# Kernel tuning notes

Measured on AMD Instinct MI355X. Metric: run time of the kernel, lower is better.

The kernel has to match this reference:

```python
import jax, jax.numpy as jnp
import numpy as np

BETA = 0.25
SK_EPSILONS = [0.0, 0.0, 0.003]
SK_ITERS = 50
B_SIZE = 262144
LATENT_DIM = 32
K = 256


def setup_inputs() -> dict:
    key = jax.random.key(0)
    kz, k0, k1, k2 = jax.random.split(key, 4)
    return {
        "z": jax.random.normal(kz, (B_SIZE, LATENT_DIM), dtype=jnp.float32),
        "cb0": jax.random.normal(k0, (K, LATENT_DIM), dtype=jnp.float32),
        "cb1": jax.random.normal(k1, (K, LATENT_DIM), dtype=jnp.float32),
        "cb2": jax.random.normal(k2, (K, LATENT_DIM), dtype=jnp.float32),
    }


def _sq_dists(residual, codebook):
    # ||r - c||^2 = ||r||^2 + ||c||^2 - 2 r.c  -> (B, K), avoids (B,K,D) broadcast
    r2 = jnp.sum(residual * residual, axis=1, keepdims=True)      # (B,1)
    c2 = jnp.sum(codebook * codebook, axis=1)                     # (K,)
    cross = residual @ codebook.T                                 # (B,K)
    return r2 + c2 - 2.0 * cross


def _sinkhorn(d_centered, epsilon, n_iters):
    # log-domain Sinkhorn-Knopp, matches torch reference
    B, Kk = d_centered.shape
    log_B = jnp.log(jnp.asarray(B, dtype=d_centered.dtype))
    log_K = jnp.log(jnp.asarray(Kk, dtype=d_centered.dtype))
    log_Q = -d_centered / epsilon
    log_Q = log_Q - jax.scipy.special.logsumexp(log_Q)

    def body(_, lq):
        lq = lq - jax.scipy.special.logsumexp(lq, axis=1, keepdims=True) - log_B
        lq = lq - jax.scipy.special.logsumexp(lq, axis=0, keepdims=True) - log_K
        return lq

    log_Q = jax.lax.fori_loop(0, n_iters, body, log_Q)
    return jnp.exp(log_Q + log_B)


def _quantize_level(residual, codebook, sk_epsilon, use_sk=True):
    dists = _sq_dists(residual, codebook)  # (B, K)
    codes_argmin = jnp.argmin(dists, axis=-1)
    if use_sk and sk_epsilon > 0:
        d = jax.lax.stop_gradient(dists)
        d_max = jnp.max(d)
        d_min = jnp.min(d)
        mid = (d_max + d_min) / 2
        amp = jnp.maximum(d_max - mid, 1e-05)
        Q = _sinkhorn((d - mid) / amp, sk_epsilon, SK_ITERS)
        bad = jnp.any(jnp.isnan(Q)) | jnp.any(jnp.isinf(Q))
        codes = jnp.where(bad, codes_argmin, jnp.argmax(Q, axis=-1))
    else:
        codes = codes_argmin
    quantized = codebook[codes]  # (B, D) gather
    return codes, quantized


def reference(z, cb0, cb1, cb2):
    codebooks = [cb0, cb1, cb2]
    sg = jax.lax.stop_gradient
    residual = z
    all_codes = []
    quantized_total = jnp.zeros_like(z)
    rq_loss = jnp.asarray(0.0, dtype=z.dtype)
    for codebook, sk_epsilon in zip(codebooks, SK_EPSILONS):
        codes, e = _quantize_level(residual, codebook, sk_epsilon, use_sk=True)
        all_codes.append(codes)
        rq_loss = rq_loss + jnp.mean((sg(residual) - e) ** 2)
        rq_loss = rq_loss + BETA * jnp.mean((residual - sg(e)) ** 2)
        e_st = residual + sg(e - residual)  # straight-through
        quantized_total = quantized_total + e_st
        residual = residual - sg(e)
    return (all_codes[0], all_codes[1], all_codes[2], quantized_total, rq_loss)
```

## Files before the change

### kernel.cpp

```cpp
#include <hip/hip_runtime.h>


#define BSZ   262144
#define DIM   32
#define KK    256
#define CHUNK 128
#define NBLK  (BSZ / CHUNK)
#define NIBLK (BSZ / 256)
#define LROW  36
#define SKEPS 0.003f
#define NIT   50

#define WS_SSQ  0
#define WS_MINK 1
#define WS_MAXK 2
#define WS_TWOT 3
#define WS_W0   256
#define WS_WA   512
#define WS_C2   1024
#define WSB_SIG 8192
#define WSB_BH  32768
#define WSB_BL  49152
#define WSB_QB  65536

#define OC0   0
#define OC1   BSZ
#define OC2   (2 * BSZ)
#define OQ    (3 * BSZ)
#define OLOSS (3 * BSZ + BSZ * DIM)
#define OU_AH (3u * BSZ)
#define OU_AL (3u * BSZ + 4194304u)

typedef short short8 __attribute__((ext_vector_type(8)));
typedef _Float16 half8 __attribute__((ext_vector_type(8)));
typedef float f32x4 __attribute__((ext_vector_type(4)));

#if __has_builtin(__builtin_amdgcn_exp2f)
#define EXP2(x) __builtin_amdgcn_exp2f(x)
#else
#define EXP2(x) exp2f(x)
#endif

#if __has_builtin(__builtin_amdgcn_update_dpp)
#define ROR16(x, N)                                                            \
  __int_as_float(__builtin_amdgcn_update_dpp(__float_as_int(x),                \
                 __float_as_int(x), 0x120 + (N), 0xF, 0xF, false))
#define ROR16I(x, N) __builtin_amdgcn_update_dpp((x), (x), 0x120 + (N), 0xF, 0xF, false)
#else
#define ROR16(x, N) __shfl_xor((x), (N))
#define ROR16I(x, N) __shfl_xor((x), (N))
#endif

__device__ __forceinline__ float wred_sum(float x) {
  x += ROR16(x, 1); x += ROR16(x, 2); x += ROR16(x, 4); x += ROR16(x, 8);
  x += __shfl_xor(x, 16); x += __shfl_xor(x, 32);
  return x;
}
__device__ __forceinline__ float wred_max(float x) {
  x = fmaxf(x, ROR16(x, 1)); x = fmaxf(x, ROR16(x, 2));
  x = fmaxf(x, ROR16(x, 4)); x = fmaxf(x, ROR16(x, 8));
  x = fmaxf(x, __shfl_xor(x, 16)); x = fmaxf(x, __shfl_xor(x, 32));
  return x;
}
__device__ __forceinline__ float wred_min(float x) {
  x = fminf(x, ROR16(x, 1)); x = fminf(x, ROR16(x, 2));
  x = fminf(x, ROR16(x, 4)); x = fminf(x, ROR16(x, 8));
  x = fminf(x, __shfl_xor(x, 16)); x = fminf(x, __shfl_xor(x, 32));
  return x;
}
__device__ __forceinline__ float g16_max(float x) {
  x = fmaxf(x, ROR16(x, 1)); x = fmaxf(x, ROR16(x, 2));
  x = fmaxf(x, ROR16(x, 4)); x = fmaxf(x, ROR16(x, 8));
  return x;
}
__device__ __forceinline__ float g16_sum(float x) {
  x += ROR16(x, 1); x += ROR16(x, 2); x += ROR16(x, 4); x += ROR16(x, 8);
  return x;
}
__device__ __forceinline__ void g16_argmax(float& v, int& j) {
  { float ov = ROR16(v,1); int oj = ROR16I(j,1); if (ov > v || (ov == v && oj < j)) { v = ov; j = oj; } }
  { float ov = ROR16(v,2); int oj = ROR16I(j,2); if (ov > v || (ov == v && oj < j)) { v = ov; j = oj; } }
  { float ov = ROR16(v,4); int oj = ROR16I(j,4); if (ov > v || (ov == v && oj < j)) { v = ov; j = oj; } }
  { float ov = ROR16(v,8); int oj = ROR16I(j,8); if (ov > v || (ov == v && oj < j)) { v = ov; j = oj; } }
}

__device__ __forceinline__ unsigned fkey(float f) {
  unsigned b = __float_as_uint(f);
  return (b & 0x80000000u) ? ~b : (b | 0x80000000u);
}
__device__ __forceinline__ float fkeyinv(unsigned k) {
  return __uint_as_float((k & 0x80000000u) ? (k ^ 0x80000000u) : ~k);
}
__device__ __forceinline__ unsigned pk2h(_Float16 a, _Float16 b) {
  unsigned short ua = __builtin_bit_cast(unsigned short, a);
  unsigned short ub = __builtin_bit_cast(unsigned short, b);
  return (unsigned)ua | ((unsigned)ub << 16);
}
__device__ __forceinline__ unsigned short bf16rne(float x) {
  unsigned u = __float_as_uint(x);
  return (unsigned short)((u + 0x7FFFu + ((u >> 16) & 1u)) >> 16);
}
__device__ __forceinline__ float bf2f(unsigned short h) {
  return __uint_as_float(((unsigned)h) << 16);
}
__device__ __forceinline__ void split3_8(const float* xs, short8& a1, short8& a2, short8& a3) {
#pragma unroll
  for (int u = 0; u < 8; ++u) {
    float x = xs[u];
    unsigned short b1 = bf16rne(x); x -= bf2f(b1);
    unsigned short b2 = bf16rne(x); x -= bf2f(b2);
    unsigned short b3 = bf16rne(x);
    a1[u] = (short)b1; a2[u] = (short)b2; a3[u] = (short)b3;
  }
}
__device__ __forceinline__ f32x4 mfma6r(short8 A1, short8 A2, short8 A3,
                                        short8 B1, short8 B2, short8 B3, f32x4 acc) {
  acc = __builtin_amdgcn_mfma_f32_16x16x32_bf16(A3, B1, acc, 0, 0, 0);
  acc = __builtin_amdgcn_mfma_f32_16x16x32_bf16(A1, B3, acc, 0, 0, 0);
  acc = __builtin_amdgcn_mfma_f32_16x16x32_bf16(A2, B2, acc, 0, 0, 0);
  acc = __builtin_amdgcn_mfma_f32_16x16x32_bf16(A2, B1, acc, 0, 0, 0);
  acc = __builtin_amdgcn_mfma_f32_16x16x32_bf16(A1, B2, acc, 0, 0, 0);
  acc = __builtin_amdgcn_mfma_f32_16x16x32_bf16(A1, B1, acc, 0, 0, 0);
  return acc;
}
__device__ __forceinline__ void build_a(const float* zl, int b, int lane,
                                        short8& A1, short8& A2, short8& A3) {
  int row = b * 16 + (lane & 15);
  int kb = (lane >> 4) * 8;
  float xs[8];
  float4 t0 = *reinterpret_cast<const float4*>(&zl[row * LROW + kb]);
  float4 t1 = *reinterpret_cast<const float4*>(&zl[row * LROW + kb + 4]);
  xs[0]=t0.x; xs[1]=t0.y; xs[2]=t0.z; xs[3]=t0.w;
  xs[4]=t1.x; xs[5]=t1.y; xs[6]=t1.z; xs[7]=t1.w;
  split3_8(xs, A1, A2, A3);
}

__global__ void prep0_k(const float* __restrict__ cb0, const float* __restrict__ cb1,
                        const float* __restrict__ cb2, unsigned* __restrict__ wsu,
                        float* __restrict__ wsf, uint4* __restrict__ qb,
                        unsigned long long* __restrict__ sig) {
  int t = threadIdx.x;
#pragma unroll
  for (int i = 0; i < 12; ++i) sig[i * 256 + t] = 0ull;
  if (t == 0) { wsu[WS_SSQ] = 0u; wsu[WS_MINK] = 0xFFFFFFFFu; wsu[WS_MAXK] = 0u; }
  const float* cbs[3] = {cb0, cb1, cb2};
  for (int lvl = 0; lvl < 3; ++lvl) {
    const float* cb = cbs[lvl];
    float s = 0.f;
#pragma unroll
    for (int d = 0; d < DIM; ++d) { float c = cb[t * DIM + d]; s = fmaf(c, c, s); }
    wsf[WS_C2 + lvl * 256 + t] = 0.5f * s;
    for (int g = 0; g < 4; ++g) {
      int slot = g * 256 + t;
      int jt = slot >> 6, l = slot & 63;
      int col = jt * 16 + (l & 15), kb = (l >> 4) * 8;
      float xs[8];
#pragma unroll
      for (int u = 0; u < 8; ++u) xs[u] = cb[col * DIM + kb + u];
      short8 b1, b2, b3;
      split3_8(xs, b1, b2, b3);
      qb[(lvl * 3 + 0) * 1024 + slot] = __builtin_bit_cast(uint4, b1);
      qb[(lvl * 3 + 1) * 1024 + slot] = __builtin_bit_cast(uint4, b2);
      qb[(lvl * 3 + 2) * 1024 + slot] = __builtin_bit_cast(uint4, b3);
    }
  }
}

__device__ __forceinline__ void loadq(uint4* dst, const uint4* __restrict__ src, int tid) {
#pragma unroll
  for (int i = 0; i < 12; ++i) dst[i * 256 + tid] = src[i * 256 + tid];
}

__device__ __forceinline__ void argmin2_lds(const uint4* qlds, const float* cini,
                                            const float* zl, int* codel, int lane, int wid) {
  short8 A1a, A2a, A3a, A1b, A2b, A3b;
  build_a(zl, wid * 2 + 0, lane, A1a, A2a, A3a);
  build_a(zl, wid * 2 + 1, lane, A1b, A2b, A3b);
  float bva[4] = {-3.4e38f, -3.4e38f, -3.4e38f, -3.4e38f};
  float bvb[4] = {-3.4e38f, -3.4e38f, -3.4e38f, -3.4e38f};
  int bja[4] = {0, 0, 0, 0}, bjb[4] = {0, 0, 0, 0};
#pragma unroll 2
  for (int jt = 0; jt < 16; ++jt) {
    float cv = cini[jt * 16 + (lane & 15)];
    short8 B1 = __builtin_bit_cast(short8, qlds[jt * 64 + lane]);
    short8 B2 = __builtin_bit_cast(short8, qlds[1024 + jt * 64 + lane]);
    short8 B3 = __builtin_bit_cast(short8, qlds[2048 + jt * 64 + lane]);
    int col = jt * 16 + (lane & 15);
    f32x4 aa = {cv, cv, cv, cv};
    aa = mfma6r(A1a, A2a, A3a, B1, B2, B3, aa);
    f32x4 ab = {cv, cv, cv, cv};
    ab = mfma6r(A1b, A2b, A3b, B1, B2, B3, ab);
#pragma unroll
    for (int r = 0; r < 4; ++r) {
      if (aa[r] > bva[r]) { bva[r] = aa[r]; bja[r] = col; }
      if (ab[r] > bvb[r]) { bvb[r] = ab[r]; bjb[r] = col; }
    }
  }
#pragma unroll
  for (int r = 0; r < 4; ++r) g16_argmax(bva[r], bja[r]);
#pragma unroll
  for (int r = 0; r < 4; ++r) g16_argmax(bvb[r], bjb[r]);
  if ((lane & 15) == 0) {
#pragma unroll
    for (int r = 0; r < 4; ++r) {
      codel[(wid * 2 + 0) * 16 + (lane >> 4) * 4 + r] = bja[r];
      codel[(wid * 2 + 1) * 16 + (lane >> 4) * 4 + r] = bjb[r];
    }
  }
}

__device__ __forceinline__ float remap_phase(const float* __restrict__ cb, float* zl,
                                             const int* codel, int tid) {
  int row = tid & (CHUNK - 1);
  int half = tid >> 7;
  const float4* cbg = reinterpret_cast<const float4*>(cb + codel[row] * DIM + half * 16);
  float4* zr = reinterpret_cast<float4*>(&zl[row * LROW + half * 16]);
  float local = 0.f;
#pragma unroll
  for (int k = 0; k < 4; ++k) {
    float4 cv = cbg[k];
    float4 v = zr[k];
    v.x -= cv.x; v.y -= cv.y; v.z -= cv.z; v.w -= cv.w;
    zr[k] = v;
    local = fmaf(v.x, v.x, local); local = fmaf(v.y, v.y, local);
    local = fmaf(v.z, v.z, local); local = fmaf(v.w, v.w, local);
  }
  return local;
}

__global__ __launch_bounds__(256, 2) void stageA_k(const float* __restrict__ z,
                                                   const float* __restrict__ cb0,
                                                   const float* __restrict__ cb1,
                                                   float* __restrict__ out,
                                                   unsigned* __restrict__ outu,
                                                   unsigned* __restrict__ wsu,
                                                   float* __restrict__ wsf,
                                                   const uint4* __restrict__ qb) {
  __shared__ float zl[CHUNK * LROW];
  __shared__ uint4 qlds[3 * 1024];
  __shared__ float c2l[256];
  __shared__ float rsq[CHUNK];
  __shared__ int codel[CHUNK];
  __shared__ float red[4];
  const int tid = threadIdx.x, lane = tid & 63, wid = tid >> 6;
  const long base = (long)blockIdx.x * CHUNK;

#pragma unroll
  for (int g = 0; g < 4; ++g) {
    int f4 = g * 256 + tid;
    float4 v = reinterpret_cast<const float4*>(z + base * DIM)[f4];
    int row = f4 >> 3, d = (f4 & 7) * 4;
    *reinterpret_cast<float4*>(&zl[row * LROW + d]) = v;
  }
  loadq(qlds, qb, tid);
  c2l[tid] = -wsf[WS_C2 + tid];
  __syncthreads();

  float loss_acc = 0.f;

  argmin2_lds(qlds, c2l, zl, codel, lane, wid);
  __syncthreads();
  if (tid < CHUNK) out[OC0 + base + tid] = (float)codel[tid];
  loss_acc += remap_phase(cb0, zl, codel, tid);
  loadq(qlds, qb + 3 * 1024, tid);
  c2l[tid] = -wsf[WS_C2 + 256 + tid];
  __syncthreads();

  argmin2_lds(qlds, c2l, zl, codel, lane, wid);
  __syncthreads();
  if (tid < CHUNK) out[OC1 + base + tid] = (float)codel[tid];
  loss_acc += remap_phase(cb1, zl, codel, tid);
  loadq(qlds, qb + 6 * 1024, tid);
  c2l[tid] = -wsf[WS_C2 + 512 + tid];
  __syncthreads();

  if (tid < CHUNK) {
    float s = 0.f;
#pragma unroll
    for (int d = 0; d < DIM; ++d) { float x = zl[tid * LROW + d]; s = fmaf(x, x, s); }
    rsq[tid] = s;
  }
  __syncthreads();

  {
    short8 A1a, A2a, A3a, A1b, A2b, A3b;
    build_a(zl, wid * 2 + 0, lane, A1a, A2a, A3a);
    build_a(zl, wid * 2 + 1, lane, A1b, A2b, A3b);
    float mna[4] = {3.4e38f, 3.4e38f, 3.4e38f, 3.4e38f};
    float mxa[4] = {-3.4e38f, -3.4e38f, -3.4e38f, -3.4e38f};
    float mnb[4] = {3.4e38f, 3.4e38f, 3.4e38f, 3.4e38f};
    float mxb[4] = {-3.4e38f, -3.4e38f, -3.4e38f, -3.4e38f};
#pragma unroll 2
    for (int jt = 0; jt < 16; ++jt) {
      float cv = c2l[jt * 16 + (lane & 15)];
      short8 B1 = __builtin_bit_cast(short8, qlds[jt * 64 + lane]);
      short8 B2 = __builtin_bit_cast(short8, qlds[1024 + jt * 64 + lane]);
      short8 B3 = __builtin_bit_cast(short8, qlds[2048 + jt * 64 + lane]);
      f32x4 aa = {cv, cv, cv, cv};
      aa = mfma6r(A1a, A2a, A3a, B1, B2, B3, aa);
      f32x4 ab = {cv, cv, cv, cv};
      ab = mfma6r(A1b, A2b, A3b, B1, B2, B3, ab);
#pragma unroll
      for (int r = 0; r < 4; ++r) {
        mna[r] = fminf(mna[r], aa[r]); mxa[r] = fmaxf(mxa[r], aa[r]);
        mnb[r] = fminf(mnb[r], ab[r]); mxb[r] = fmaxf(mxb[r], ab[r]);
      }
    }
    float dmn = 3.4e38f, dmx = -3.4e38f;
#pragma unroll
    for (int r = 0; r < 4; ++r) {
      float r2a = rsq[(wid * 2 + 0) * 16 + (lane >> 4) * 4 + r];
      float r2b = rsq[(wid * 2 + 1) * 16 + (lane >> 4) * 4 + r];
      dmn = fminf(dmn, fminf(fmaf(-2.f, mxa[r], r2a), fmaf(-2.f, mxb[r], r2b)));
      dmx = fmaxf(dmx, fmaxf(fmaf(-2.f, mna[r], r2a), fmaf(-2.f, mnb[r], r2b)));
    }
    dmn = wred_min(dmn);
    dmx = wred_max(dmx);
    if (lane == 0) {
      atomicMin(&wsu[WS_MINK], fkey(dmn));
      atomicMax(&wsu[WS_MAXK], fkey(dmx));
    }
  }

#pragma unroll
  for (int g2 = 0; g2 < 8; ++g2) {
    int slot = g2 * 256 + tid;
    int b = slot >> 8;
    int l = (slot >> 2) & 63;
    int u = slot & 3;
    int row = b * 16 + (l & 15);
    int k = (l >> 4) * 8 + u * 2;
    float x0 = zl[row * LROW + k], x1 = zl[row * LROW + k + 1];
    _Float16 h0 = (_Float16)x0, h1 = (_Float16)x1;
    _Float16 q0 = (_Float16)(x0 - (float)h0), q1 = (_Float16)(x1 - (float)h1);
    unsigned gbase = ((unsigned)blockIdx.x * 8u + (unsigned)b) * 256u + (unsigned)(l * 4 + u);
    outu[OU_AH + gbase] = pk2h(h0, h1);
    outu[OU_AL + gbase] = pk2h(q0, q1);
  }

  loss_acc = wred_sum(loss_acc);
  if (lane == 0) red[wid] = loss_acc;
  __syncthreads();
  if (tid == 0) atomicAdd(&wsf[WS_SSQ], red[0] + red[1] + red[2] + red[3]);
}

__global__ void prep_k(const float* __restrict__ cb2, unsigned* __restrict__ wsu,
                       float* __restrict__ wsf, unsigned* __restrict__ bh,
                       unsigned* __restrict__ bl, uint4* __restrict__ qb) {
  int j = threadIdx.x;
  float dmin = fkeyinv(wsu[WS_MINK]);
  float dmax = fkeyinv(wsu[WS_MAXK]);
  float mid = (dmax + dmin) * 0.5f;
  float amp = fmaxf(dmax - mid, 1e-5f);
  float t = 1.0f / (amp * SKEPS);
  const float L2E = 1.4426950408889634f;
  float T2L = 2.0f * t * L2E;
  if (j == 0) wsf[WS_TWOT] = T2L;
  float s = 0.f;
#pragma unroll
  for (int d = 0; d < DIM; ++d) { float c = cb2[j * DIM + d]; s = fmaf(c, c, s); }
  wsf[WS_W0 + j] = -t * L2E * s;
  for (int g = 0; g < 16; ++g) {
    int slot = g * 256 + j;
    int jt = slot >> 8, l = (slot >> 2) & 63, u = slot & 3;
    int col = jt * 16 + (l & 15);
    int k = (l >> 4) * 8 + u * 2;
    float b0 = T2L * cb2[col * DIM + k], b1 = T2L * cb2[col * DIM + k + 1];
    _Float16 h0 = (_Float16)b0, h1 = (_Float16)b1;
    _Float16 q0 = (_Float16)(b0 - (float)h0), q1 = (_Float16)(b1 - (float)h1);
    bh[slot] = pk2h(h0, h1);
    bl[slot] = pk2h(q0, q1);
  }
  for (int g = 0; g < 4; ++g) {
    int slot = g * 256 + j;
    int jt = slot >> 6, l = slot & 63;
    int col = jt * 16 + (l & 15), kb = (l >> 4) * 8;
    float xs[8];
#pragma unroll
    for (int u = 0; u < 8; ++u) xs[u] = T2L * cb2[col * DIM + kb + u];
    short8 b1v, b2v, b3v;
    split3_8(xs, b1v, b2v, b3v);
    qb[9 * 1024 + slot]  = __builtin_bit_cast(uint4, b1v);
    qb[10 * 1024 + slot] = __builtin_bit_cast(uint4, b2v);
    qb[11 * 1024 + slot] = __builtin_bit_cast(uint4, b3v);
  }
}

__global__ __launch_bounds__(256, 4) void iter_k(const uint4* __restrict__ afh,
                                                 const uint4* __restrict__ afl,
                                                 const uint4* __restrict__ bfh,
                                                 const uint4* __restrict__ bfl,
                                                 const float* __restrict__ w_rd,
                                                 float* __restrict__ w_wr,
                                                 const unsigned long long* __restrict__ s_rd,
                                                 unsigned long long* __restrict__ s_wr,
                                                 unsigned long long* __restrict__ s_zr,
                                                 int first) {
  __shared__ uint4 Blo[1024];
  __shared__ float wsh[KK];
  __shared__ float exm[8][2][2][16];
  __shared__ float exs[8][2][2][16];
  __shared__ float ssh[2][KK];
  const int tid = threadIdx.x, lane = tid & 63, wv = tid >> 6;
  const int pair = wv >> 1, ch = wv & 1, g = lane >> 4;

  {
    unsigned long long tt = s_rd[tid] + s_rd[256 + tid] + s_rd[512 + tid] + s_rd[768 + tid];
    float wj = first ? w_rd[tid]
                     : w_rd[tid] + 34.0f - log2f(fmaxf((float)tt, 1.0f));
    wsh[tid] = wj;
    if (blockIdx.x == 0) {
      w_wr[tid] = wj;
      s_zr[tid] = 0ull; s_zr[256 + tid] = 0ull;
      s_zr[512 + tid] = 0ull; s_zr[768 + tid] = 0ull;
    }
  }
#pragma unroll
  for (int i = 0; i < 4; ++i) Blo[i * 256 + tid] = bfl[i * 256 + tid];
  half8 Bh[8];
#pragma unroll
  for (int jt = 0; jt < 8; ++jt)
    Bh[jt] = __builtin_bit_cast(half8, bfh[(ch * 8 + jt) * 64 + lane]);
  __syncthreads();
  float wc[8];
#pragma unroll
  for (int c = 0; c < 8; ++c) wc[c] = wsh[(ch * 8 + c) * 16 + (lane & 15)];

  float sg[8] = {0.f, 0.f, 0.f, 0.f, 0.f, 0.f, 0.f, 0.f};

#pragma unroll 1
  for (int b = 0; b < 8; ++b) {
    const int batchid = blockIdx.x * 16 + pair * 8 + b;
    half8 Ah = __builtin_bit_cast(half8, afh[batchid * 64 + lane]);
    half8 Al = __builtin_bit_cast(half8, afl[batchid * 64 + lane]);
    f32x4 v[8];
#pragma unroll
    for (int jt = 0; jt < 8; ++jt) {
      half8 Blv = __builtin_bit_cast(half8, Blo[(ch * 8 + jt) * 64 + lane]);
      f32x4 acc = {wc[jt], wc[jt], wc[jt], wc[jt]};
      acc = __builtin_amdgcn_mfma_f32_16x16x32_f16(Al, Bh[jt], acc, 0, 0, 0);
      acc = __builtin_amdgcn_mfma_f32_16x16x32_f16(Ah, Blv, acc, 0, 0, 0);
      acc = __builtin_amdgcn_mfma_f32_16x16x32_f16(Ah, Bh[jt], acc, 0, 0, 0);
      v[jt] = acc;
    }
    float m[4];
#pragma unroll
    for (int r = 0; r < 4; ++r) {
      float a01 = fmaxf(v[0][r], v[1][r]), a23 = fmaxf(v[2][r], v[3][r]);
      float a45 = fmaxf(v[4][r], v[5][r]), a67 = fmaxf(v[6][r], v[7][r]);
      m[r] = g16_max(fmaxf(fmaxf(a01, a23), fmaxf(a45, a67)));
    }
    float s[4];
#pragma unroll
    for (int r = 0; r < 4; ++r) {
#pragma unroll
      for (int jt = 0; jt < 8; ++jt) v[jt][r] = EXP2(v[jt][r] - m[r]);
      float s01 = v[0][r] + v[1][r], s23 = v[2][r] + v[3][r];
      float s45 = v[4][r] + v[5][r], s67 = v[6][r] + v[7][r];
      s[r] = g16_sum((s01 + s23) + (s45 + s67));
    }
    if ((lane & 15) == 0) {
      *reinterpret_cast<float4*>(&exm[b][pair][ch][g * 4]) = make_float4(m[0], m[1], m[2], m[3]);
      *reinterpret_cast<float4*>(&exs[b][pair][ch][g * 4]) = make_float4(s[0], s[1], s[2], s[3]);
    }
    __syncthreads();
    float4 pm = *reinterpret_cast<const float4*>(&exm[b][pair][ch ^ 1][g * 4]);
    float4 ps = *reinterpret_cast<const float4*>(&exs[b][pair][ch ^ 1][g * 4]);
    float rinv[4];
    {
      float pmv[4] = {pm.x, pm.y, pm.z, pm.w};
      float psv[4] = {ps.x, ps.y, ps.z, ps.w};
#pragma unroll
      for (int r = 0; r < 4; ++r) {
        float M = fmaxf(m[r], pmv[r]);
        float sc = EXP2(m[r] - M);
        float tot = fmaf(s[r], sc, psv[r] * EXP2(pmv[r] - M));
        rinv[r] = sc * __builtin_amdgcn_rcpf(tot);
      }
    }
#pragma unroll
    for (int jt = 0; jt < 8; ++jt)
#pragma unroll
      for (int r = 0; r < 4; ++r) sg[jt] = fmaf(v[jt][r], rinv[r], sg[jt]);
  }
#pragma unroll
  for (int jt = 0; jt < 8; ++jt) {
    float x = sg[jt];
    x += __shfl_xor(x, 16); x += __shfl_xor(x, 32);
    sg[jt] = x;
  }
  if (lane < 16) {
#pragma unroll
    for (int jt = 0; jt < 8; ++jt) ssh[pair][ch * 128 + jt * 16 + lane] = sg[jt];
  }
  __syncthreads();
  float stot = ssh[0][tid] + ssh[1][tid];
  atomicAdd(s_wr + (blockIdx.x & 3) * 256 + tid,
            (unsigned long long)fmaf(stot, 16777216.0f, 0.5f));
}

__global__ __launch_bounds__(256, 2) void final_k(const float* __restrict__ z,
                                                  const float* __restrict__ cb0,
                                                  const float* __restrict__ cb1,
                                                  const float* __restrict__ cb2,
                                                  float* __restrict__ out,
                                                  float* __restrict__ wssq,
                                                  const uint4* __restrict__ qb,
                                                  const float* __restrict__ w_rd,
                                                  const unsigned long long* __restrict__ s_rd) {
  __shared__ float zl[CHUNK * LROW];
  __shared__ uint4 qlds[3 * 1024];
  __shared__ float wsh[KK];
  __shared__ int codel[CHUNK];
  __shared__ float red[4];
  const int tid = threadIdx.x, lane = tid & 63, wid = tid >> 6;
  const long base = (long)blockIdx.x * CHUNK;

  {
    unsigned long long tt = s_rd[tid] + s_rd[256 + tid] + s_rd[512 + tid] + s_rd[768 + tid];
    wsh[tid] = w_rd[tid] + 34.0f - log2f(fmaxf((float)tt, 1.0f));
  }
  loadq(qlds, qb + 9 * 1024, tid);
#pragma unroll
  for (int g = 0; g < 4; ++g) {
    int f4 = g * 256 + tid;
    float4 v = reinterpret_cast<const float4*>(z + base * DIM)[f4];
    int row = f4 >> 3, d = (f4 & 7) * 4;
    *reinterpret_cast<float4*>(&zl[row * LROW + d]) = v;
  }
  __syncthreads();
  {
    int row = tid & (CHUNK - 1);
    int half = tid >> 7;
    int c0 = (int)out[OC0 + base + row];
    int c1 = (int)out[OC1 + base + row];
    const float4* e0 = reinterpret_cast<const float4*>(cb0 + c0 * DIM + half * 16);
    const float4* e1 = reinterpret_cast<const float4*>(cb1 + c1 * DIM + half * 16);
    float4* zr = reinterpret_cast<float4*>(&zl[row * LROW + half * 16]);
#pragma unroll
    for (int k = 0; k < 4; ++k) {
      float4 a = e0[k], bb = e1[k], v = zr[k];
      v.x = (v.x - a.x) - bb.x; v.y = (v.y - a.y) - bb.y;
      v.z = (v.z - a.z) - bb.z; v.w = (v.w - a.w) - bb.w;
      zr[k] = v;
    }
  }
  __syncthreads();

  argmin2_lds(qlds, wsh, zl, codel, lane, wid);
  __syncthreads();
  if (tid < CHUNK) out[OC2 + base + tid] = (float)codel[tid];

  float loss_acc = 0.f;
#pragma unroll
  for (int g = 0; g < 4; ++g) {
    int f4 = g * 256 + tid;
    int row = f4 >> 3, d = (f4 & 7) * 4;
    float4 e = *reinterpret_cast<const float4*>(cb2 + codel[row] * DIM + d);
    float4 r = *reinterpret_cast<const float4*>(&zl[row * LROW + d]);
    float4 zv = reinterpret_cast<const float4*>(z + base * DIM)[f4];
    float4 q;
    q.x = zv.x - r.x + e.x; q.y = zv.y - r.y + e.y;
    q.z = zv.z - r.z + e.z; q.w = zv.w - r.w + e.w;
    reinterpret_cast<float4*>(out + OQ + base * DIM)[f4] = q;
    float rx = r.x - e.x, ry = r.y - e.y, rz = r.z - e.z, rw = r.w - e.w;
    loss_acc = fmaf(rx, rx, loss_acc); loss_acc = fmaf(ry, ry, loss_acc);
    loss_acc = fmaf(rz, rz, loss_acc); loss_acc = fmaf(rw, rw, loss_acc);
  }
  loss_acc = wred_sum(loss_acc);
  if (lane == 0) red[wid] = loss_acc;
  __syncthreads();
  if (tid == 0) atomicAdd(&wssq[WS_SSQ], red[0] + red[1] + red[2] + red[3]);
}

__global__ void losswrite_k(float* __restrict__ out, const float* __restrict__ wsf) {
  if (threadIdx.x == 0) out[OLOSS] = 1.25f * wsf[WS_SSQ] / 8388608.0f;
}

extern "C" void kernel_launch(void* const* d_in, const int* in_sizes, int n_in,
                              void* d_out, int out_size, void* d_ws, size_t ws_size,
                              hipStream_t stream) {
  const float* z   = (const float*)d_in[0];
  const float* cb0 = (const float*)d_in[1];
  const float* cb1 = (const float*)d_in[2];
  const float* cb2 = (const float*)d_in[3];
  float* out = (float*)d_out;
  unsigned* outu = (unsigned*)d_out;
  float* wsf = (float*)d_ws;
  unsigned* wsu = (unsigned*)d_ws;
  unsigned long long* sig = (unsigned long long*)((char*)d_ws + WSB_SIG);
  unsigned* bh = (unsigned*)((char*)d_ws + WSB_BH);
  unsigned* bl = (unsigned*)((char*)d_ws + WSB_BL);
  uint4* qb = (uint4*)((char*)d_ws + WSB_QB);

  const uint4* afh = (const uint4*)(outu + OU_AH);
  const uint4* afl = (const uint4*)(outu + OU_AL);
  const uint4* bfh = (const uint4*)bh;
  const uint4* bfl = (const uint4*)bl;

  prep0_k<<<1, 256, 0, stream>>>(cb0, cb1, cb2, wsu, wsf, qb, sig);
  stageA_k<<<NBLK, 256, 0, stream>>>(z, cb0, cb1, out, outu, wsu, wsf, qb);
  prep_k<<<1, 256, 0, stream>>>(cb2, wsu, wsf, bh, bl, qb);
  for (int it = 0; it < NIT; ++it) {
    const float* w_rd = (it == 0) ? (wsf + WS_W0) : (wsf + WS_WA + ((it - 1) & 1) * KK);
    float* w_wr = wsf + WS_WA + (it & 1) * KK;
    const unsigned long long* s_rd = sig + 1024 * ((it + 2) % 3);
    unsigned long long* s_wr = sig + 1024 * (it % 3);
    unsigned long long* s_zr = sig + 1024 * ((it + 1) % 3);
    iter_k<<<NIBLK, 256, 0, stream>>>(afh, afl, bfh, bfl, w_rd, w_wr, s_rd, s_wr, s_zr,
                                      it == 0 ? 1 : 0);
  }
  final_k<<<NBLK, 256, 0, stream>>>(z, cb0, cb1, cb2, out, wsf, qb,
                                    wsf + WS_WA + ((NIT - 1) & 1) * KK,
                                    sig + 1024 * ((NIT - 1) % 3));
  losswrite_k<<<1, 64, 0, stream>>>(out, wsf);
}
```

Baseline: 1.963 ms.

## Fuse Sinkhorn iterations into one persistent cooperative kernel with grid sync

Adds a cooperative persistent kernel that runs all 50 Sinkhorn iterations in one launch. Blocks loop over batch chunks and meet at a grid-wide barrier after each iteration's column-sum atomics. The dual weights stay in registers, and the codebook fragments are loaded once instead of once per launch. This is meant to remove the launch and tail gaps of 50 separate kernel launches. In exchange it pays a grid.sync per iteration and relies on the cooperative launch succeeding, falling back to the old per-iteration launches if it does not.

Result: slower. 4.290 ms (+118.5%).

```diff
diff --git a/kernel.cpp b/kernel.cpp
--- a/kernel.cpp
+++ b/kernel.cpp
@@ -1,4 +1,7 @@
 #include <hip/hip_runtime.h>
+#include <hip/hip_cooperative_groups.h>
+
+namespace cg = cooperative_groups;
 
 
 #define BSZ   262144
@@ -386,6 +389,133 @@
   }
 }
 
+__device__ __forceinline__ void sink_body(int chunk, int pair, int ch, int g, int lane,
+                                          const uint4* __restrict__ afh,
+                                          const uint4* __restrict__ afl,
+                                          const half8 Bh[8], const uint4* Blo,
+                                          const float wc[8], float sg[8],
+                                          float (*exm)[2][2][16], float (*exs)[2][2][16]) {
+#pragma unroll 1
+  for (int b = 0; b < 8; ++b) {
+    const int batchid = chunk * 16 + pair * 8 + b;
+    half8 Ah = __builtin_bit_cast(half8, afh[batchid * 64 + lane]);
+    half8 Al = __builtin_bit_cast(half8, afl[batchid * 64 + lane]);
+    f32x4 v[8];
+#pragma unroll
+    for (int jt = 0; jt < 8; ++jt) {
+      half8 Blv = __builtin_bit_cast(half8, Blo[(ch * 8 + jt) * 64 + lane]);
+      f32x4 acc = {wc[jt], wc[jt], wc[jt], wc[jt]};
+      acc = __builtin_amdgcn_mfma_f32_16x16x32_f16(Al, Bh[jt], acc, 0, 0, 0);
+      acc = __builtin_amdgcn_mfma_f32_16x16x32_f16(Ah, Blv, acc, 0, 0, 0);
+      acc = __builtin_amdgcn_mfma_f32_16x16x32_f16(Ah, Bh[jt], acc, 0, 0, 0);
+      v[jt] = acc;
+    }
+    float m[4];
+#pragma unroll
+    for (int r = 0; r < 4; ++r) {
+      float a01 = fmaxf(v[0][r], v[1][r]), a23 = fmaxf(v[2][r], v[3][r]);
+      float a45 = fmaxf(v[4][r], v[5][r]), a67 = fmaxf(v[6][r], v[7][r]);
+      m[r] = g16_max(fmaxf(fmaxf(a01, a23), fmaxf(a45, a67)));
+    }
+    float s[4];
+#pragma unroll
+    for (int r = 0; r < 4; ++r) {
+#pragma unroll
+      for (int jt = 0; jt < 8; ++jt) v[jt][r] = EXP2(v[jt][r] - m[r]);
+      float s01 = v[0][r] + v[1][r], s23 = v[2][r] + v[3][r];
+      float s45 = v[4][r] + v[5][r], s67 = v[6][r] + v[7][r];
+      s[r] = g16_sum((s01 + s23) + (s45 + s67));
+    }
+    if ((lane & 15) == 0) {
+      *reinterpret_cast<float4*>(&exm[b][pair][ch][g * 4]) = make_float4(m[0], m[1], m[2], m[3]);
+      *reinterpret_cast<float4*>(&exs[b][pair][ch][g * 4]) = make_float4(s[0], s[1], s[2], s[3]);
+    }
+    __syncthreads();
+    float4 pm = *reinterpret_cast<const float4*>(&exm[b][pair][ch ^ 1][g * 4]);
+    float4 ps = *reinterpret_cast<const float4*>(&exs[b][pair][ch ^ 1][g * 4]);
+    float rinv[4];
+    {
+      float pmv[4] = {pm.x, pm.y, pm.z, pm.w};
+      float psv[4] = {ps.x, ps.y, ps.z, ps.w};
+#pragma unroll
+      for (int r = 0; r < 4; ++r) {
+        float M = fmaxf(m[r], pmv[r]);
+        float sc = EXP2(m[r] - M);
+        float tot = fmaf(s[r], sc, psv[r] * EXP2(pmv[r] - M));
+        rinv[r] = sc * __builtin_amdgcn_rcpf(tot);
+      }
+    }
+#pragma unroll
+    for (int jt = 0; jt < 8; ++jt)
+#pragma unroll
+      for (int r = 0; r < 4; ++r) sg[jt] = fmaf(v[jt][r], rinv[r], sg[jt]);
+  }
+}
+
+__global__ __launch_bounds__(256, 4) void sink_k(const uint4* __restrict__ afh,
+                                                 const uint4* __restrict__ afl,
+                                                 const uint4* __restrict__ bfh,
+                                                 const uint4* __restrict__ bfl,
+                                                 const float* __restrict__ w0,
+                                                 float* __restrict__ wfin,
+                                                 unsigned long long* __restrict__ sig) {
+  cg::grid_group grid = cg::this_grid();
+  __shared__ uint4 Blo[1024];
+  __shared__ float wsh[KK];
+  __shared__ float exm[8][2][2][16];
+  __shared__ float exs[8][2][2][16];
+  __shared__ float ssh[2][KK];
+  const int tid = threadIdx.x, lane = tid & 63, wv = tid >> 6;
+  const int pair = wv >> 1, ch = wv & 1, g = lane >> 4;
+
+#pragma unroll
+  for (int i = 0; i < 4; ++i) Blo[i * 256 + tid] = bfl[i * 256 + tid];
+  half8 Bh[8];
+#pragma unroll
+  for (int jt = 0; jt < 8; ++jt)
+    Bh[jt] = __builtin_bit_cast(half8, bfh[(ch * 8 + jt) * 64 + lane]);
+  float w_reg = w0[tid];
+
+#pragma unroll 1
+  for (int it = 0; it < NIT; ++it) {
+    const unsigned long long* s_rd = sig + 1024 * ((it + 2) % 3);
+    unsigned long long* s_wr = sig + 1024 * (it % 3);
+    unsigned long long* s_zr = sig + 1024 * ((it + 1) % 3);
+    if (it > 0) {
+      unsigned long long tt = s_rd[tid] + s_rd[256 + tid] + s_rd[512 + tid] + s_rd[768 + tid];
+      w_reg += 34.0f - log2f(fmaxf((float)tt, 1.0f));
+    }
+    wsh[tid] = w_reg;
+    if (blockIdx.x < 4) s_zr[(int)blockIdx.x * 256 + tid] = 0ull;
+    __syncthreads();
+    float wc[8];
+#pragma unroll
+    for (int c = 0; c < 8; ++c) wc[c] = wsh[(ch * 8 + c) * 16 + (lane & 15)];
+    float sg[8] = {0.f, 0.f, 0.f, 0.f, 0.f, 0.f, 0.f, 0.f};
+
+#pragma unroll 1
+    for (int chunk = blockIdx.x; chunk < NIBLK; chunk += gridDim.x)
+      sink_body(chunk, pair, ch, g, lane, afh, afl, Bh, Blo, wc, sg, exm, exs);
+
+#pragma unroll
+    for (int jt = 0; jt < 8; ++jt) {
+      float x = sg[jt];
+      x += __shfl_xor(x, 16); x += __shfl_xor(x, 32);
+      sg[jt] = x;
+    }
+    if (lane < 16) {
+#pragma unroll
+      for (int jt = 0; jt < 8; ++jt) ssh[pair][ch * 128 + jt * 16 + lane] = sg[jt];
+    }
+    __syncthreads();
+    float stot = ssh[0][tid] + ssh[1][tid];
+    atomicAdd(s_wr + ((int)blockIdx.x & 3) * 256 + tid,
+              (unsigned long long)fmaf(stot, 16777216.0f, 0.5f));
+    grid.sync();
+  }
+  if (blockIdx.x == 0) wfin[tid] = w_reg;
+}
+
 __global__ __launch_bounds__(256, 4) void iter_k(const uint4* __restrict__ afh,
                                                  const uint4* __restrict__ afl,
                                                  const uint4* __restrict__ bfh,
@@ -425,64 +555,10 @@
   float wc[8];
 #pragma unroll
   for (int c = 0; c < 8; ++c) wc[c] = wsh[(ch * 8 + c) * 16 + (lane & 15)];
-
   float sg[8] = {0.f, 0.f, 0.f, 0.f, 0.f, 0.f, 0.f, 0.f};
 
-#pragma unroll 1
-  for (int b = 0; b < 8; ++b) {
-    const int batchid = blockIdx.x * 16 + pair * 8 + b;
-    half8 Ah = __builtin_bit_cast(half8, afh[batchid * 64 + lane]);
-    half8 Al = __builtin_bit_cast(half8, afl[batchid * 64 + lane]);
-    f32x4 v[8];
-#pragma unroll
-    for (int jt = 0; jt < 8; ++jt) {
-      half8 Blv = __builtin_bit_cast(half8, Blo[(ch * 8 + jt) * 64 + lane]);
-      f32x4 acc = {wc[jt], wc[jt], wc[jt], wc[jt]};
-      acc = __builtin_amdgcn_mfma_f32_16x16x32_f16(Al, Bh[jt], acc, 0, 0, 0);
-      acc = __builtin_amdgcn_mfma_f32_16x16x32_f16(Ah, Blv, acc, 0, 0, 0);
-      acc = __builtin_amdgcn_mfma_f32_16x16x32_f16(Ah, Bh[jt], acc, 0, 0, 0);
-      v[jt] = acc;
-    }
-    float m[4];
-#pragma unroll
-    for (int r = 0; r < 4; ++r) {
-      float a01 = fmaxf(v[0][r], v[1][r]), a23 = fmaxf(v[2][r], v[3][r]);
-      float a45 = fmaxf(v[4][r], v[5][r]), a67 = fmaxf(v[6][r], v[7][r]);
-      m[r] = g16_max(fmaxf(fmaxf(a01, a23), fmaxf(a45, a67)));
-    }
-    float s[4];
-#pragma unroll
-    for (int r = 0; r < 4; ++r) {
-#pragma unroll
-      for (int jt = 0; jt < 8; ++jt) v[jt][r] = EXP2(v[jt][r] - m[r]);
-      float s01 = v[0][r] + v[1][r], s23 = v[2][r] + v[3][r];
-      float s45 = v[4][r] + v[5][r], s67 = v[6][r] + v[7][r];
-      s[r] = g16_sum((s01 + s23) + (s45 + s67));
-    }
-    if ((lane & 15) == 0) {
-      *reinterpret_cast<float4*>(&exm[b][pair][ch][g * 4]) = make_float4(m[0], m[1], m[2], m[3]);
-      *reinterpret_cast<float4*>(&exs[b][pair][ch][g * 4]) = make_float4(s[0], s[1], s[2], s[3]);
-    }
-    __syncthreads();
-    float4 pm = *reinterpret_cast<const float4*>(&exm[b][pair][ch ^ 1][g * 4]);
-    float4 ps = *reinterpret_cast<const float4*>(&exs[b][pair][ch ^ 1][g * 4]);
-    float rinv[4];
-    {
-      float pmv[4] = {pm.x, pm.y, pm.z, pm.w};
-      float psv[4] = {ps.x, ps.y, ps.z, ps.w};
-#pragma unroll
-      for (int r = 0; r < 4; ++r) {
-        float M = fmaxf(m[r], pmv[r]);
-        float sc = EXP2(m[r] - M);
-        float tot = fmaf(s[r], sc, psv[r] * EXP2(pmv[r] - M));
-        rinv[r] = sc * __builtin_amdgcn_rcpf(tot);
-      }
-    }
-#pragma unroll
-    for (int jt = 0; jt < 8; ++jt)
-#pragma unroll
-      for (int r = 0; r < 4; ++r) sg[jt] = fmaf(v[jt][r], rinv[r], sg[jt]);
-  }
+  sink_body(blockIdx.x, pair, ch, g, lane, afh, afl, Bh, Blo, wc, sg, exm, exs);
+
 #pragma unroll
   for (int jt = 0; jt < 8; ++jt) {
     float x = sg[jt];
@@ -597,21 +673,42 @@
   const uint4* afl = (const uint4*)(outu + OU_AL);
   const uint4* bfh = (const uint4*)bh;
   const uint4* bfl = (const uint4*)bl;
+  const float* w0p = wsf + WS_W0;
+  float* wfin = wsf + WS_WA;
 
   prep0_k<<<1, 256, 0, stream>>>(cb0, cb1, cb2, wsu, wsf, qb, sig);
   stageA_k<<<NBLK, 256, 0, stream>>>(z, cb0, cb1, out, outu, wsu, wsf, qb);
   prep_k<<<1, 256, 0, stream>>>(cb2, wsu, wsf, bh, bl, qb);
-  for (int it = 0; it < NIT; ++it) {
-    const float* w_rd = (it == 0) ? (wsf + WS_W0) : (wsf + WS_WA + ((it - 1) & 1) * KK);
-    float* w_wr = wsf + WS_WA + (it & 1) * KK;
-    const unsigned long long* s_rd = sig + 1024 * ((it + 2) % 3);
-    unsigned long long* s_wr = sig + 1024 * (it % 3);
-    unsigned long long* s_zr = sig + 1024 * ((it + 1) % 3);
-    iter_k<<<NIBLK, 256, 0, stream>>>(afh, afl, bfh, bfl, w_rd, w_wr, s_rd, s_wr, s_zr,
-                                      it == 0 ? 1 : 0);
+
+  bool coop = false;
+  {
+    int maxb = 0;
+    if (hipOccupancyMaxActiveBlocksPerMultiprocessor(&maxb, (const void*)sink_k, 256, 0)
+            == hipSuccess && maxb >= 1) {
+      int sgrid = maxb * 256;
+      if (sgrid > NIBLK) sgrid = NIBLK;
+      unsigned long long* sigp = sig;
+      void* args[] = {(void*)&afh, (void*)&afl, (void*)&bfh, (void*)&bfl,
+                      (void*)&w0p, (void*)&wfin, (void*)&sigp};
+      if (hipLaunchCooperativeKernel((void*)sink_k, dim3(sgrid), dim3(256), args, 0,
+                                     stream) == hipSuccess)
+        coop = true;
+    }
+  }
+  const float* w_last = wfin;
+  if (!coop) {
+    for (int it = 0; it < NIT; ++it) {
+      const float* w_rd = (it == 0) ? (wsf + WS_W0) : (wsf + WS_WA + ((it - 1) & 1) * KK);
+      float* w_wr = wsf + WS_WA + (it & 1) * KK;
+      const unsigned long long* s_rd = sig + 1024 * ((it + 2) % 3);
+      unsigned long long* s_wr = sig + 1024 * (it % 3);
+      unsigned long long* s_zr = sig + 1024 * ((it + 1) % 3);
+      iter_k<<<NIBLK, 256, 0, stream>>>(afh, afl, bfh, bfl, w_rd, w_wr, s_rd, s_wr, s_zr,
+                                        it == 0 ? 1 : 0);
+    }
+    w_last = wsf + WS_WA + ((NIT - 1) & 1) * KK;
   }
   final_k<<<NBLK, 256, 0, stream>>>(z, cb0, cb1, cb2, out, wsf, qb,
-                                    wsf + WS_WA + ((NIT - 1) & 1) * KK,
-                                    sig + 1024 * ((NIT - 1) % 3));
+                                    w_last, sig + 1024 * ((NIT - 1) % 3));
   losswrite_k<<<1, 64, 0, stream>>>(out, wsf);
 }
```
